# Optimization experiments

Hardware: AMD Instinct MI355X
Metric: run time of the kernel (lower is better)

The kernel has to match this reference:

```python
import jax, jax.numpy as jnp
import numpy as np

D_IN = 2048
NUM_HEADS = 16
QK_NOPE = 64
QK_ROPE = 64
QK_HEAD = QK_NOPE + QK_ROPE  # 128
V_HEAD = 128
KV_LORA = 1024
SEQ = 4096
BATCH = 1
SCALE = QK_HEAD ** -0.5
EPS = 1e-6


def rmsnorm(x, w):
    return x * jax.lax.rsqrt(jnp.mean(x * x, axis=-1, keepdims=True) + EPS) * w


def apply_rope(x, cos, sin):
    # x: [B, S, H, D]; cos/sin: [S, D//2]; pairs are consecutive elements (view_as_complex)
    b, s, h, d = x.shape
    xr = x.reshape(b, s, h, d // 2, 2)
    xe, xo = xr[..., 0], xr[..., 1]
    c = cos[None, :, None, :]
    sn = sin[None, :, None, :]
    oe = xe * c - xo * sn
    oo = xe * sn + xo * c
    return jnp.stack([oe, oo], axis=-1).reshape(b, s, h, d)


def setup_inputs() -> dict:
    key = jax.random.key(0)
    ks = jax.random.split(key, 8)
    x = jax.random.normal(ks[0], (BATCH, SEQ, D_IN), dtype=jnp.float32)
    # rotary tables (rope_theta=10000)
    inv_freq = 1.0 / (10000.0 ** (np.arange(0, QK_ROPE, 2, dtype=np.float32) / QK_ROPE))
    angles = np.arange(SEQ, dtype=np.float32)[:, None] * inv_freq[None, :]
    cos = jnp.asarray(np.cos(angles), dtype=jnp.float32)
    sin = jnp.asarray(np.sin(angles), dtype=jnp.float32)
    # causal additive mask [S, S]
    mask = jnp.where(jnp.triu(jnp.ones((SEQ, SEQ), dtype=bool), k=1), -1e9, 0.0).astype(jnp.float32)
    def lin(k, fan_out, fan_in):
        bound = 1.0 / np.sqrt(fan_in)
        return jax.random.uniform(k, (fan_out, fan_in), jnp.float32, -bound, bound)
    wq = lin(ks[1], NUM_HEADS * QK_HEAD, D_IN)
    wkv_a = lin(ks[2], KV_LORA + QK_ROPE, D_IN)
    kv_norm_w = jnp.ones((KV_LORA,), dtype=jnp.float32)
    wkv_b = lin(ks[3], NUM_HEADS * (QK_NOPE + V_HEAD), KV_LORA)
    wo = lin(ks[4], D_IN, NUM_HEADS * V_HEAD)
    return {"x": x, "cos": cos, "sin": sin, "mask": mask, "wq": wq,
            "wkv_a": wkv_a, "kv_norm_w": kv_norm_w, "wkv_b": wkv_b, "wo": wo,
            "start_pos": 0}


def reference(x, cos, sin, mask, wq, wkv_a, kv_norm_w, wkv_b, wo, start_pos):
    b, s, _ = x.shape
    # Q projection -> [B, S, H, qk_head_dim]
    q = (x @ wq.T).reshape(b, s, NUM_HEADS, QK_HEAD)
    q_nope, q_pe = q[..., :QK_NOPE], q[..., QK_NOPE:]
    q_pe = apply_rope(q_pe, cos, sin)
    # KV low-rank projection
    kv_full = x @ wkv_a.T                               # [B, S, KV_LORA + QK_ROPE]
    kv, k_pe = kv_full[..., :KV_LORA], kv_full[..., KV_LORA:]
    k_pe = apply_rope(k_pe[:, :, None, :], cos, sin)    # [B, S, 1, QK_ROPE]
    # naive path: expand latent to per-head k_nope / v
    q = jnp.concatenate([q_nope, q_pe], axis=-1)        # [B, S, H, 128]
    kvb = (rmsnorm(kv, kv_norm_w) @ wkv_b.T).reshape(b, s, NUM_HEADS, QK_NOPE + V_HEAD)
    k_nope, v = kvb[..., :QK_NOPE], kvb[..., QK_NOPE:]
    k = jnp.concatenate([k_nope, jnp.broadcast_to(k_pe, (b, s, NUM_HEADS, QK_ROPE))], axis=-1)
    # start_pos=0 prefill: cache[:, :end_pos] == freshly written k, v
    scores = jnp.einsum('bqhd,bkhd->bqhk', q, k) * SCALE  # [B, S, H, S]
    scores = scores + mask[None, :, None, :]
    probs = jax.nn.softmax(scores.astype(jnp.float32), axis=-1).astype(x.dtype)
    out = jnp.einsum('bqhk,bkhd->bqhd', probs, v)       # [B, S, H, V_HEAD]
    return out.reshape(b, s, NUM_HEADS * V_HEAD) @ wo.T
```

## Files before the change

### kernel.cpp

```cpp
#include <hip/hip_runtime.h>

typedef __bf16 bf16;
typedef __attribute__((ext_vector_type(8))) __bf16 bf16x8;
typedef __attribute__((ext_vector_type(2))) __bf16 bf16x2;
typedef __attribute__((ext_vector_type(4))) float f32x4;
typedef __attribute__((ext_vector_type(4))) int int4v;

typedef __attribute__((address_space(1))) const void gconst_t;
typedef __attribute__((address_space(3))) void lvoid_t;

#define SEQ 4096
#define D_IN 2048
#define NHEADS 16
#define QSCALE (0.08838834764831843f * 1.4426950408889634f)
#define RMS_EPS 1e-6f
#define QKV_N 3136

__device__ inline unsigned pack2bf(float a, float b) {
    bf16x2 t; t[0] = (bf16)a; t[1] = (bf16)b;
    return __builtin_bit_cast(unsigned, t);
}

__device__ inline void conv_seg(const float* __restrict__ in, bf16* __restrict__ out,
                                int n, int i0, int stride) {
    for (int i = i0; i < n; i += stride) {
        float4 v = *reinterpret_cast<const float4*>(in + i);
        bf16 o[4];
        o[0] = (bf16)v.x; o[1] = (bf16)v.y; o[2] = (bf16)v.z; o[3] = (bf16)v.w;
        *reinterpret_cast<uint2*>(out + i) = *reinterpret_cast<uint2*>(o);
    }
}

__global__ __launch_bounds__(256) void convert_all_kernel(
    const float* __restrict__ xs,  const float* __restrict__ wqs,
    const float* __restrict__ was, const float* __restrict__ wbs,
    const float* __restrict__ wos,
    bf16* __restrict__ xd, bf16* __restrict__ wqd, bf16* __restrict__ wad,
    bf16* __restrict__ wbd, bf16* __restrict__ wod) {
    int i0 = (blockIdx.x * 256 + threadIdx.x) * 4;
    int stride = gridDim.x * 256 * 4;
    conv_seg(xs,  xd,  4096 * 2048, i0, stride);
    conv_seg(wqs, wqd, 2048 * 2048, i0, stride);
    conv_seg(was, wad, 1088 * 2048, i0, stride);
    conv_seg(wbs, wbd, 3072 * 1024, i0, stride);
    conv_seg(wos, wod, 2048 * 2048, i0, stride);
}

template<int BN, bool BF16_OUT>
__global__ __launch_bounds__(512, 2) void gemm256_kernel(
    const bf16* __restrict__ A, const bf16* __restrict__ B, void* __restrict__ Cout,
    int M, int N, int K) {
    constexpr int CB = BN / 64;
    constexpr int NF = BN / 64;
    constexpr int WC = BN / 4;
    __shared__ __align__(16) bf16 Al[2][256 * 64];
    __shared__ __align__(16) bf16 Bl[2][BN * 64];

    int t    = threadIdx.x;
    int lane = t & 63;
    int w    = t >> 6;
    int wr   = w >> 2;
    int wc   = w & 3;
    int l15  = lane & 15;
    int g    = lane >> 4;
    int m0 = blockIdx.y * 256;
    int n0 = blockIdx.x * BN;

    f32x4 acc[8][NF] = {};

    auto stage = [&](int kt, int buf) {
        int k0 = kt << 6;
        #pragma unroll
        for (int c = 0; c < 4; c++) {
            int idx = c * 512 + t;
            int r = idx >> 3;
            int u = (idx & 7) ^ (r & 7);
            const bf16* ga = A + (size_t)(m0 + r) * K + k0 + u * 8;
            __builtin_amdgcn_global_load_lds((gconst_t*)ga,
                (lvoid_t*)&Al[buf][(c * 512 + w * 64) * 8], 16, 0, 0);
        }
        #pragma unroll
        for (int c = 0; c < CB; c++) {
            int idx = c * 512 + t;
            int r = idx >> 3;
            int u = (idx & 7) ^ (r & 7);
            int br = n0 + r; if (br >= N) br = N - 1;
            const bf16* gb = B + (size_t)br * K + k0 + u * 8;
            __builtin_amdgcn_global_load_lds((gconst_t*)gb,
                (lvoid_t*)&Bl[buf][(c * 512 + w * 64) * 8], 16, 0, 0);
        }
    };

    int nt = K >> 6;
    stage(0, 0);
    for (int kt = 0; kt < nt; ++kt) {
        int buf = kt & 1;
        if (kt + 1 < nt) {
            stage(kt + 1, buf ^ 1);
            __builtin_amdgcn_sched_barrier(0);
            if constexpr (BN == 256) asm volatile("s_waitcnt vmcnt(8)" ::: "memory");
            else                     asm volatile("s_waitcnt vmcnt(6)" ::: "memory");
            __builtin_amdgcn_sched_barrier(0);
        } else {
            __builtin_amdgcn_sched_barrier(0);
            asm volatile("s_waitcnt vmcnt(0)" ::: "memory");
            __builtin_amdgcn_sched_barrier(0);
        }
        __builtin_amdgcn_s_barrier();

        #pragma unroll
        for (int ks = 0; ks < 2; ++ks) {
            bf16x8 af[8], bfv[NF];
            #pragma unroll
            for (int mt = 0; mt < 8; mt++) {
                int ra = wr * 128 + mt * 16 + l15;
                int u = (ks * 4 + g) ^ (ra & 7);
                af[mt] = *reinterpret_cast<const bf16x8*>(&Al[buf][ra * 64 + u * 8]);
            }
            #pragma unroll
            for (int nf = 0; nf < NF; nf++) {
                int rb = wc * WC + nf * 16 + l15;
                int u = (ks * 4 + g) ^ (rb & 7);
                bfv[nf] = *reinterpret_cast<const bf16x8*>(&Bl[buf][rb * 64 + u * 8]);
            }
            __builtin_amdgcn_s_setprio(1);
            #pragma unroll
            for (int mt = 0; mt < 8; mt++)
                #pragma unroll
                for (int nf = 0; nf < NF; nf++)
                    acc[mt][nf] = __builtin_amdgcn_mfma_f32_16x16x32_bf16(af[mt], bfv[nf], acc[mt][nf], 0, 0, 0);
            __builtin_amdgcn_s_setprio(0);
        }
        __builtin_amdgcn_s_barrier();
    }

    #pragma unroll
    for (int mt = 0; mt < 8; mt++) {
        #pragma unroll
        for (int nf = 0; nf < NF; nf++) {
            int col = n0 + wc * WC + nf * 16 + l15;
            if (col < N) {
                #pragma unroll
                for (int r = 0; r < 4; r++) {
                    int row = m0 + wr * 128 + mt * 16 + g * 4 + r;
                    if (BF16_OUT)
                        ((bf16*)Cout)[(size_t)row * N + col] = (bf16)acc[mt][nf][r];
                    else
                        ((float*)Cout)[(size_t)row * N + col] = acc[mt][nf][r];
                }
            }
        }
    }
}

__global__ __launch_bounds__(256) void prep_q_kernel(
    bf16* __restrict__ qkv, const float* __restrict__ cosb, const float* __restrict__ sinb) {
    int s = blockIdx.x;
    int t = threadIdx.x;
    bf16* p = qkv + (size_t)s * QKV_N + t * 8;
    bf16x8 v = *reinterpret_cast<bf16x8*>(p);
    float f[8];
    #pragma unroll
    for (int j = 0; j < 8; j++) f[j] = (float)v[j];
    int d0 = (t & 15) * 8;
    if (d0 >= 64) {
        int ib = (d0 - 64) >> 1;
        #pragma unroll
        for (int pr = 0; pr < 4; pr++) {
            float c  = cosb[s * 32 + ib + pr];
            float sn = sinb[s * 32 + ib + pr];
            float xe = f[pr*2], xo = f[pr*2 + 1];
            f[pr*2]     = xe * c - xo * sn;
            f[pr*2 + 1] = xe * sn + xo * c;
        }
    }
    #pragma unroll
    for (int j = 0; j < 8; j++) v[j] = (bf16)(f[j] * QSCALE);
    *reinterpret_cast<bf16x8*>(p) = v;
}

__global__ __launch_bounds__(256) void prep_kv_kernel(
    const bf16* __restrict__ qkv, const float* __restrict__ w,
    const float* __restrict__ cosb, const float* __restrict__ sinb,
    bf16* __restrict__ kvnorm, bf16* __restrict__ kpe) {
    __shared__ float red[4];
    int s = blockIdx.x;
    int t = threadIdx.x;
    const bf16* src = qkv + (size_t)s * QKV_N + 2048;
    float f[4];
    {
        uint2 raw = *reinterpret_cast<const uint2*>(src + t * 4);
        bf16* vb = reinterpret_cast<bf16*>(&raw);
        float ss = 0.f;
        #pragma unroll
        for (int j = 0; j < 4; j++) { f[j] = (float)vb[j]; ss += f[j] * f[j]; }
        #pragma unroll
        for (int m = 1; m < 64; m <<= 1) ss += __shfl_xor(ss, m);
        if ((t & 63) == 0) red[t >> 6] = ss;
    }
    __syncthreads();
    float tot = red[0] + red[1] + red[2] + red[3];
    float rms = rsqrtf(tot * (1.0f / 1024.0f) + RMS_EPS);
    bf16 o[4];
    #pragma unroll
    for (int j = 0; j < 4; j++) o[j] = (bf16)(f[j] * rms * w[t*4 + j]);
    *reinterpret_cast<uint2*>(kvnorm + (size_t)s * 1024 + t * 4) = *reinterpret_cast<uint2*>(o);
    if (t < 16) {
        float e[4];
        #pragma unroll
        for (int j = 0; j < 4; j++) e[j] = (float)src[1024 + t*4 + j];
        int ib = t * 2;
        float c0 = cosb[s*32 + ib],     s0 = sinb[s*32 + ib];
        float c1 = cosb[s*32 + ib + 1], s1 = sinb[s*32 + ib + 1];
        bf16 ko[4];
        ko[0] = (bf16)(e[0]*c0 - e[1]*s0);
        ko[1] = (bf16)(e[0]*s0 + e[1]*c0);
        ko[2] = (bf16)(e[2]*c1 - e[3]*s1);
        ko[3] = (bf16)(e[2]*s1 + e[3]*c1);
        *reinterpret_cast<uint2*>(kpe + (size_t)s * 64 + t * 4) = *reinterpret_cast<uint2*>(ko);
    }
}

__global__ __launch_bounds__(256) void build_vt_kernel(
    const bf16* __restrict__ kvb, bf16* __restrict__ vt) {
    const int LT = 130;
    __shared__ bf16 lt[64 * 130];
    int h  = blockIdx.y;
    int s0 = blockIdx.x * 64;
    int t  = threadIdx.x;
    {
        int row = t >> 2;
        int d0  = (t & 3) * 32;
        const bf16* src = kvb + (size_t)(s0 + row) * 3072 + h * 192 + 64 + d0;
        int4v v0 = *reinterpret_cast<const int4v*>(src);
        int4v v1 = *reinterpret_cast<const int4v*>(src + 8);
        int4v v2 = *reinterpret_cast<const int4v*>(src + 16);
        int4v v3 = *reinterpret_cast<const int4v*>(src + 24);
        int* dst = reinterpret_cast<int*>(&lt[row * LT + d0]);
        int* s0p = reinterpret_cast<int*>(&v0); int* s1p = reinterpret_cast<int*>(&v1);
        int* s2p = reinterpret_cast<int*>(&v2); int* s3p = reinterpret_cast<int*>(&v3);
        #pragma unroll
        for (int j = 0; j < 4; j++) { dst[j] = s0p[j]; dst[4+j] = s1p[j]; dst[8+j] = s2p[j]; dst[12+j] = s3p[j]; }
    }
    __syncthreads();
    int ss = t & 63;
    int db = t >> 6;
    bf16* out = vt + (size_t)h * 128 * 4096 + s0 + ss;
    #pragma unroll
    for (int dd = db; dd < 128; dd += 4)
        out[(size_t)dd * 4096] = lt[ss * LT + dd];
}

__global__ __launch_bounds__(256, 2) void attn_kernel(
    const bf16* __restrict__ q,
    const bf16* __restrict__ kvb,
    const bf16* __restrict__ kpe,
    const bf16* __restrict__ vt,
    bf16* __restrict__ attn) {
    const int LPS = 72;
    __shared__ __align__(16) bf16 Kl[2][64 * 128];
    __shared__ __align__(16) bf16 Vl[2][128 * 64];
    __shared__ __align__(16) bf16 Pl[4][16 * 72];
    __shared__ __align__(16) float bcast[4][16];

    int h    = blockIdx.y;
    int tile = (h < 8) ? (31 - (int)blockIdx.x) : (int)blockIdx.x;
    int q0   = tile * 128;
    int t  = threadIdx.x;
    int lane = t & 63;
    int w  = t >> 6;
    int l15 = lane & 15;
    int g   = lane >> 4;
    int sw  = l15 & 7;
    int qrow = q0 + w * 32;

    const bf16* kvbh = kvb + h * 192;
    const bf16* vth  = vt + (size_t)h * 524288;

    bf16x8 qf[2][4];
    #pragma unroll
    for (int mt = 0; mt < 2; mt++) {
        const bf16* qp = q + (size_t)(qrow + mt*16 + l15) * QKV_N + h * 128 + g * 8;
        #pragma unroll
        for (int c = 0; c < 4; c++) qf[mt][c] = *reinterpret_cast<const bf16x8*>(qp + c * 32);
    }
    asm volatile("s_waitcnt vmcnt(0)" ::: "memory");

    f32x4 o[2][8] = {};
    float mrow[2], lrow[2];
    #pragma unroll
    for (int mt = 0; mt < 2; mt++) { mrow[mt] = -3e38f; lrow[mt] = 0.f; }

    int nch = (q0 >> 6) + 2;
    int dc  = (q0 >> 6) + (w >> 1);

    auto stageK = [&](int jc, int buf) {
        int j0 = jc << 6;
        #pragma unroll
        for (int c = 0; c < 4; c++) {
            int idx = c*256 + w*64 + lane;
            int row = idx >> 4;
            int u   = (idx & 15) ^ (row & 7);
            const bf16* src = (u < 8)
                ? kvbh + (size_t)(j0 + row) * 3072 + u * 8
                : kpe  + (size_t)(j0 + row) * 64  + (u - 8) * 8;
            __builtin_amdgcn_global_load_lds((gconst_t*)src,
                (lvoid_t*)&Kl[buf][(c*256 + w*64) * 8], 16, 0, 0);
        }
    };
    auto stageV = [&](int jc, int buf) {
        int j0 = jc << 6;
        #pragma unroll
        for (int c = 0; c < 4; c++) {
            int idx = c*256 + w*64 + lane;
            int row = idx >> 3;
            int u   = (idx & 7) ^ (row & 7);
            const bf16* src = vth + (size_t)row * 4096 + j0 + u * 8;
            __builtin_amdgcn_global_load_lds((gconst_t*)src,
                (lvoid_t*)&Vl[buf][(c*256 + w*64) * 8], 16, 0, 0);
        }
    };

    stageK(0, 0); stageV(0, 0);

    for (int jc = 0; jc < nch; ++jc) {
        if (jc + 1 < nch) {
            stageK(jc + 1, (jc + 1) & 1); stageV(jc + 1, (jc + 1) & 1);
            __builtin_amdgcn_sched_barrier(0);
            asm volatile("s_waitcnt vmcnt(8)" ::: "memory");
            __builtin_amdgcn_sched_barrier(0);
        } else {
            __builtin_amdgcn_sched_barrier(0);
            asm volatile("s_waitcnt vmcnt(0)" ::: "memory");
            __builtin_amdgcn_sched_barrier(0);
        }
        __builtin_amdgcn_s_barrier();

        if (jc <= dc) {
            int cur = jc & 1;
            int j0  = jc << 6;
            bool masked = (jc == dc);

            f32x4 sfr[2][4];
            __builtin_amdgcn_s_setprio(1);
            #pragma unroll
            for (int s = 0; s < 4; ++s) {
                int krow = s*16 + l15;
                bf16x8 kf[4];
                #pragma unroll
                for (int c = 0; c < 4; ++c)
                    kf[c] = *reinterpret_cast<const bf16x8*>(
                        &Kl[cur][krow*128 + (((c*4 + g) ^ sw) * 8)]);
                #pragma unroll
                for (int mt = 0; mt < 2; ++mt) {
                    f32x4 acc = {};
                    acc = __builtin_amdgcn_mfma_f32_16x16x32_bf16(kf[0], qf[mt][0], acc, 0, 0, 0);
                    acc = __builtin_amdgcn_mfma_f32_16x16x32_bf16(kf[1], qf[mt][1], acc, 0, 0, 0);
                    acc = __builtin_amdgcn_mfma_f32_16x16x32_bf16(kf[2], qf[mt][2], acc, 0, 0, 0);
                    acc = __builtin_amdgcn_mfma_f32_16x16x32_bf16(kf[3], qf[mt][3], acc, 0, 0, 0);
                    sfr[mt][s] = acc;
                }
            }
            __builtin_amdgcn_s_setprio(0);

            bf16x8 pf[2][2];
            #pragma unroll
            for (int mt = 0; mt < 2; ++mt) {
                int i = qrow + mt*16 + l15;
                if (masked) {
                    #pragma unroll
                    for (int s = 0; s < 4; ++s)
                        #pragma unroll
                        for (int r = 0; r < 4; ++r) {
                            int j = j0 + s*16 + g*4 + r;
                            if (j > i) sfr[mt][s][r] = -3e38f;
                        }
                }
                float m01 = fmaxf(fmaxf(sfr[mt][0][0], sfr[mt][0][1]),
                                  fmaxf(sfr[mt][0][2], sfr[mt][0][3]));
                float m23 = fmaxf(fmaxf(sfr[mt][1][0], sfr[mt][1][1]),
                                  fmaxf(sfr[mt][1][2], sfr[mt][1][3]));
                float m45 = fmaxf(fmaxf(sfr[mt][2][0], sfr[mt][2][1]),
                                  fmaxf(sfr[mt][2][2], sfr[mt][2][3]));
                float m67 = fmaxf(fmaxf(sfr[mt][3][0], sfr[mt][3][1]),
                                  fmaxf(sfr[mt][3][2], sfr[mt][3][3]));
                float mloc = fmaxf(fmaxf(m01, m23), fmaxf(m45, m67));
                float mx = fmaxf(mloc, __shfl_xor(mloc, 16));
                mx = fmaxf(mx, __shfl_xor(mx, 32));
                bool need = mx > mrow[mt];
                float mnew = fmaxf(mrow[mt], mx);
                float sfac = __builtin_amdgcn_exp2f(mrow[mt] - mnew);
                mrow[mt] = mnew;
                float psum = 0.f;
                #pragma unroll
                for (int s = 0; s < 4; ++s)
                    #pragma unroll
                    for (int r = 0; r < 4; ++r) {
                        float p = __builtin_amdgcn_exp2f(sfr[mt][s][r] - mnew);
                        sfr[mt][s][r] = p;
                        psum += p;
                    }
                lrow[mt] = lrow[mt] * sfac + psum;
                #pragma unroll
                for (int s = 0; s < 4; ++s) {
                    unsigned u0 = pack2bf(sfr[mt][s][0], sfr[mt][s][1]);
                    unsigned u1 = pack2bf(sfr[mt][s][2], sfr[mt][s][3]);
                    *reinterpret_cast<unsigned*>(&Pl[w][l15 * LPS + s*16 + g*4])     = u0;
                    *reinterpret_cast<unsigned*>(&Pl[w][l15 * LPS + s*16 + g*4 + 2]) = u1;
                }
                if (g == 0) bcast[w][l15] = sfac;
                f32x4 sf4 = *reinterpret_cast<const f32x4*>(&bcast[w][g*4]);
                if (__any(need)) {
                    #pragma unroll
                    for (int dt = 0; dt < 8; ++dt)
                        #pragma unroll
                        for (int r = 0; r < 4; ++r) o[mt][dt][r] *= sf4[r];
                }
                pf[mt][0] = *reinterpret_cast<const bf16x8*>(&Pl[w][l15 * LPS + g * 8]);
                pf[mt][1] = *reinterpret_cast<const bf16x8*>(&Pl[w][l15 * LPS + 32 + g * 8]);
            }

            __builtin_amdgcn_s_setprio(1);
            #pragma unroll
            for (int dt = 0; dt < 8; ++dt) {
                int vrow = dt*16 + l15;
                bf16x8 va = *reinterpret_cast<const bf16x8*>(
                    &Vl[cur][vrow*64 + ((g ^ sw) * 8)]);
                bf16x8 vb = *reinterpret_cast<const bf16x8*>(
                    &Vl[cur][vrow*64 + (((4 + g) ^ sw) * 8)]);
                o[0][dt] = __builtin_amdgcn_mfma_f32_16x16x32_bf16(pf[0][0], va, o[0][dt], 0, 0, 0);
                o[0][dt] = __builtin_amdgcn_mfma_f32_16x16x32_bf16(pf[0][1], vb, o[0][dt], 0, 0, 0);
                o[1][dt] = __builtin_amdgcn_mfma_f32_16x16x32_bf16(pf[1][0], va, o[1][dt], 0, 0, 0);
                o[1][dt] = __builtin_amdgcn_mfma_f32_16x16x32_bf16(pf[1][1], vb, o[1][dt], 0, 0, 0);
            }
            __builtin_amdgcn_s_setprio(0);
        }
        __builtin_amdgcn_s_barrier();
    }

    #pragma unroll
    for (int mt = 0; mt < 2; ++mt) {
        float l = lrow[mt];
        l += __shfl_xor(l, 16);
        l += __shfl_xor(l, 32);
        float linv = __builtin_amdgcn_rcpf(l);
        if (g == 0) bcast[w][l15] = linv;
        f32x4 li4 = *reinterpret_cast<const f32x4*>(&bcast[w][g*4]);
        #pragma unroll
        for (int r = 0; r < 4; ++r) {
            int i = qrow + mt*16 + g*4 + r;
            #pragma unroll
            for (int dt = 0; dt < 8; ++dt)
                attn[(size_t)i * 2048 + h * 128 + dt*16 + l15] = (bf16)(o[mt][dt][r] * li4[r]);
        }
    }
}

extern "C" void kernel_launch(void* const* d_in, const int* in_sizes, int n_in,
                              void* d_out, int out_size, void* d_ws, size_t ws_size,
                              hipStream_t stream) {
    const float* x    = (const float*)d_in[0];
    const float* cosb = (const float*)d_in[1];
    const float* sinb = (const float*)d_in[2];
    const float* wq   = (const float*)d_in[4];
    const float* wkva = (const float*)d_in[5];
    const float* kvw  = (const float*)d_in[6];
    const float* wkvb = (const float*)d_in[7];
    const float* wo   = (const float*)d_in[8];

    char* ws = (char*)d_ws;
    bf16* x_bf    = (bf16*)(ws + 0);
    bf16* kvnorm  = (bf16*)(ws + 0);
    bf16* attn    = (bf16*)(ws + 0);
    bf16* wq_bf   = (bf16*)(ws + 16777216);
    bf16* wkva_bf = (bf16*)(ws + 25165824);
    bf16* wkvb_bf = (bf16*)(ws + 29622272);
    bf16* wo_bf   = (bf16*)(ws + 35913728);
    bf16* qkv     = (bf16*)(ws + 44302336);
    bf16* kpe     = (bf16*)(ws + 69992448);
    bf16* kvb     = (bf16*)(ws + 70516736);
    bf16* vt      = (bf16*)(ws + 95682560);

    convert_all_kernel<<<dim3(2048), dim3(256), 0, stream>>>(
        x, wq, wkva, wkvb, wo, x_bf, wq_bf, wkva_bf, wkvb_bf, wo_bf);

    gemm256_kernel<256, true><<<dim3(13, 16), dim3(512), 0, stream>>>(x_bf, wq_bf, qkv, 4096, QKV_N, 2048);

    prep_q_kernel <<<dim3(4096), dim3(256), 0, stream>>>(qkv, cosb, sinb);
    prep_kv_kernel<<<dim3(4096), dim3(256), 0, stream>>>(qkv, kvw, cosb, sinb, kvnorm, kpe);

    gemm256_kernel<256, true><<<dim3(12, 16), dim3(512), 0, stream>>>(kvnorm, wkvb_bf, kvb, 4096, 3072, 1024);

    build_vt_kernel<<<dim3(64, 16), dim3(256), 0, stream>>>(kvb, vt);

    attn_kernel<<<dim3(32, 16), dim3(256), 0, stream>>>(qkv, kvb, kpe, vt, attn);

    gemm256_kernel<128, false><<<dim3(16, 16), dim3(512), 0, stream>>>(attn, wo_bf, (float*)d_out, 4096, 2048, 2048);
}
```

Measured before the change: 336.5 us.

## Read V directly from global memory in attention and raise occupancy

```diff
diff --git a/kernel.cpp b/kernel.cpp
--- a/kernel.cpp
+++ b/kernel.cpp
@@ -251,7 +251,7 @@
         out[(size_t)dd * 4096] = lt[ss * LT + dd];
 }
 
-__global__ __launch_bounds__(256, 2) void attn_kernel(
+__global__ __launch_bounds__(256, 3) void attn_kernel(
     const bf16* __restrict__ q,
     const bf16* __restrict__ kvb,
     const bf16* __restrict__ kpe,
@@ -259,7 +259,6 @@
     bf16* __restrict__ attn) {
     const int LPS = 72;
     __shared__ __align__(16) bf16 Kl[2][64 * 128];
-    __shared__ __align__(16) bf16 Vl[2][128 * 64];
     __shared__ __align__(16) bf16 Pl[4][16 * 72];
     __shared__ __align__(16) float bcast[4][16];
 
@@ -284,7 +283,6 @@
         #pragma unroll
         for (int c = 0; c < 4; c++) qf[mt][c] = *reinterpret_cast<const bf16x8*>(qp + c * 32);
     }
-    asm volatile("s_waitcnt vmcnt(0)" ::: "memory");
 
     f32x4 o[2][8] = {};
     float mrow[2], lrow[2];
@@ -308,33 +306,12 @@
                 (lvoid_t*)&Kl[buf][(c*256 + w*64) * 8], 16, 0, 0);
         }
     };
-    auto stageV = [&](int jc, int buf) {
-        int j0 = jc << 6;
-        #pragma unroll
-        for (int c = 0; c < 4; c++) {
-            int idx = c*256 + w*64 + lane;
-            int row = idx >> 3;
-            int u   = (idx & 7) ^ (row & 7);
-            const bf16* src = vth + (size_t)row * 4096 + j0 + u * 8;
-            __builtin_amdgcn_global_load_lds((gconst_t*)src,
-                (lvoid_t*)&Vl[buf][(c*256 + w*64) * 8], 16, 0, 0);
-        }
-    };
-
-    stageK(0, 0); stageV(0, 0);
+
+    stageK(0, 0);
 
     for (int jc = 0; jc < nch; ++jc) {
-        if (jc + 1 < nch) {
-            stageK(jc + 1, (jc + 1) & 1); stageV(jc + 1, (jc + 1) & 1);
-            __builtin_amdgcn_sched_barrier(0);
-            asm volatile("s_waitcnt vmcnt(8)" ::: "memory");
-            __builtin_amdgcn_sched_barrier(0);
-        } else {
-            __builtin_amdgcn_sched_barrier(0);
-            asm volatile("s_waitcnt vmcnt(0)" ::: "memory");
-            __builtin_amdgcn_sched_barrier(0);
-        }
-        __builtin_amdgcn_s_barrier();
+        __syncthreads();
+        if (jc + 1 < nch) stageK(jc + 1, (jc + 1) & 1);
 
         if (jc <= dc) {
             int cur = jc & 1;
@@ -423,11 +400,9 @@
             __builtin_amdgcn_s_setprio(1);
             #pragma unroll
             for (int dt = 0; dt < 8; ++dt) {
-                int vrow = dt*16 + l15;
-                bf16x8 va = *reinterpret_cast<const bf16x8*>(
-                    &Vl[cur][vrow*64 + ((g ^ sw) * 8)]);
-                bf16x8 vb = *reinterpret_cast<const bf16x8*>(
-                    &Vl[cur][vrow*64 + (((4 + g) ^ sw) * 8)]);
+                const bf16* vp = vth + (size_t)(dt*16 + l15) * 4096 + j0 + g * 8;
+                bf16x8 va = *reinterpret_cast<const bf16x8*>(vp);
+                bf16x8 vb = *reinterpret_cast<const bf16x8*>(vp + 32);
                 o[0][dt] = __builtin_amdgcn_mfma_f32_16x16x32_bf16(pf[0][0], va, o[0][dt], 0, 0, 0);
                 o[0][dt] = __builtin_amdgcn_mfma_f32_16x16x32_bf16(pf[0][1], vb, o[0][dt], 0, 0, 0);
                 o[1][dt] = __builtin_amdgcn_mfma_f32_16x16x32_bf16(pf[1][0], va, o[1][dt], 0, 0, 0);
@@ -435,7 +410,6 @@
             }
             __builtin_amdgcn_s_setprio(0);
         }
-        __builtin_amdgcn_s_barrier();
     }
 
     #pragma unroll
```

New measurement: 635.8 us. 1.89x slower.
